# Performance work log

Measured on AMD Instinct MI355X. Metric: run time of the kernel, lower is better.

The kernel has to match this reference:

```python
import jax, jax.numpy as jnp
import numpy as np

B, M, N, C = 8192, 16, 256, 64


def setup_inputs() -> dict:
    key = jax.random.key(0)
    k1, k2 = jax.random.split(key)
    inputs = jax.random.normal(k1, (B, M, C), dtype=jnp.float32)
    codebook = jax.random.normal(k2, (M, N, C), dtype=jnp.float32)
    return {"inputs": inputs, "codebook": codebook}


def reference(inputs, codebook):
    # inputs: [B, M, C]; codebook: [M, N, C]
    # (avoids materializing the torch [B, M, N, C] broadcast difference)
    x2 = jnp.sum(inputs * inputs, axis=-1)[:, :, None]          # [B, M, 1]
    c2 = jnp.sum(codebook * codebook, axis=-1)[None, :, :]      # [1, M, N]
    xc = jnp.einsum('bmc,mnc->bmn', inputs, codebook)           # [B, M, N]
    dist = x2 - 2.0 * xc + c2                                   # [B, M, N]
    idx = jnp.argmin(dist, axis=-1)                             # [B, M] int
    m_idx = jnp.arange(codebook.shape[0])[None, :]              # [1, M]
    codes = codebook[m_idx, idx]                                # [B, M, C]
    return codes, idx
```

## Files before the change

### kernel.cpp

```cpp
#include <hip/hip_runtime.h>
#include <hip/hip_bf16.h>
#include <float.h>


#define BQ 8192
#define MQ 16
#define NQ 256
#define CQ 64
#define RPB 512

typedef short  shortx8 __attribute__((ext_vector_type(8)));
typedef float  f32x4   __attribute__((ext_vector_type(4)));

#define HI_MASK 0xffff0000u

__device__ __forceinline__ void split3_pair(float a, float b,
                                            uint& q0, uint& q1, uint& q2) {
    const uint ba = __builtin_bit_cast(uint, a);
    const uint bb = __builtin_bit_cast(uint, b);
    q0 = (ba >> 16) | (bb & HI_MASK);
    const float r1a = a - __builtin_bit_cast(float, ba & HI_MASK);
    const float r1b = b - __builtin_bit_cast(float, bb & HI_MASK);
    const uint c1a = __builtin_bit_cast(uint, r1a);
    const uint c1b = __builtin_bit_cast(uint, r1b);
    q1 = (c1a >> 16) | (c1b & HI_MASK);
    const float r2a = r1a - __builtin_bit_cast(float, c1a & HI_MASK);
    const float r2b = r1b - __builtin_bit_cast(float, c1b & HI_MASK);
    q2 = (__builtin_bit_cast(uint, r2a) >> 16) |
         (__builtin_bit_cast(uint, r2b) & HI_MASK);
}

__global__ __launch_bounds__(1024, 4) void fq_fused_kernel(
        const float* __restrict__ inputs,
        const float* __restrict__ codebook,
        float* __restrict__ out_codes,
        float* __restrict__ out_idx) {
    const int m    = blockIdx.y;
    const int rowB = blockIdx.x * RPB;
    const int w    = (int)threadIdx.x >> 6;
    const int lane = (int)threadIdx.x & 63;
    const int quad = lane >> 4;
    const int col  = lane & 15;

    __shared__ unsigned short lds_b[96 * 512];
    __shared__ float s_c2v[NQ];

    const float* cbm = codebook + (size_t)m * NQ * CQ;
    #pragma unroll
    for (int it = 0; it < 2; ++it) {
        const int item = (int)threadIdx.x + it * 1024;
        const int kc = item & 7;
        const int n  = item >> 3;
        const int nt = n >> 4, cc = n & 15;
        const int h = kc >> 2, q = kc & 3;
        const float* src = cbm + (size_t)n * CQ + kc * 8;
        const float4 va = *(const float4*)src;
        const float4 vb = *(const float4*)(src + 4);
        const float el[8] = {va.x, va.y, va.z, va.w, vb.x, vb.y, vb.z, vb.w};

        float s = 0.0f;
        #pragma unroll
        for (int u = 0; u < 8; ++u) s = fmaf(el[u], el[u], s);
        s += __shfl_xor(s, 1, 64);
        s += __shfl_xor(s, 2, 64);
        s += __shfl_xor(s, 4, 64);
        if (kc == 0) s_c2v[n] = s;

        uint p0[4], p1[4], p2[4];
        #pragma unroll
        for (int u = 0; u < 4; ++u)
            split3_pair(el[2 * u], el[2 * u + 1], p0[u], p1[u], p2[u]);
        const int lf = q * 16 + cc;
        #pragma unroll
        for (int j = 0; j < 3; ++j) {
            const uint* p = (j == 0) ? p0 : (j == 1) ? p1 : p2;
            unsigned short* dst =
                &lds_b[(((j << 1) + h) * 16 + nt) * 512 + lf * 8];
            *(uint4*)dst = make_uint4(p[0], p[1], p[2], p[3]);
        }
    }
    __syncthreads();

    #pragma unroll 1
    for (int tt = 0; tt < 2; ++tt) {
        const int row0 = rowB + w * 32 + tt * 16;

        const float* xb = inputs + ((size_t)(row0 + col) * MQ + m) * CQ;
        shortx8 afr[3][2];
        #pragma unroll
        for (int h = 0; h < 2; ++h) {
            const float4 va = *(const float4*)(xb + h * 32 + quad * 8);
            const float4 vb = *(const float4*)(xb + h * 32 + quad * 8 + 4);
            const float el[8] = {va.x, va.y, va.z, va.w, vb.x, vb.y, vb.z, vb.w};
            uint q0[4], q1[4], q2[4];
            #pragma unroll
            for (int u = 0; u < 4; ++u)
                split3_pair(el[2 * u], el[2 * u + 1], q0[u], q1[u], q2[u]);
            afr[0][h] = __builtin_bit_cast(shortx8,
                make_uint4(q0[0], q0[1], q0[2], q0[3]));
            afr[1][h] = __builtin_bit_cast(shortx8,
                make_uint4(q1[0], q1[1], q1[2], q1[3]));
            afr[2][h] = __builtin_bit_cast(shortx8,
                make_uint4(q2[0], q2[1], q2[2], q2[3]));
        }

        float bd0[4]; int bi0[4];
        #pragma unroll 1
        for (int chh = 0; chh < 2; ++chh) {
            float c2r[8];
            #pragma unroll
            for (int nt = 0; nt < 8; ++nt)
                c2r[nt] = s_c2v[chh * 128 + nt * 16 + col];

            f32x4 acc[8];
            #pragma unroll
            for (int nt = 0; nt < 8; ++nt)
                acc[nt] = (f32x4){0.f, 0.f, 0.f, 0.f};

            #pragma unroll
            for (int h = 0; h < 2; ++h) {
                #pragma unroll
                for (int j = 0; j < 3; ++j) {
                    shortx8 bfr[8];
                    #pragma unroll
                    for (int nt = 0; nt < 8; ++nt)
                        bfr[nt] = *(const shortx8*)
                            &lds_b[(((j << 1) + h) * 16 + chh * 8 + nt) * 512
                                   + lane * 8];
                    #pragma unroll
                    for (int i = 0; i <= 2 - j; ++i) {
                        #pragma unroll
                        for (int nt = 0; nt < 8; ++nt)
                            acc[nt] = __builtin_amdgcn_mfma_f32_16x16x32_bf16(
                                afr[i][h], bfr[nt], acc[nt], 0, 0, 0);
                    }
                }
            }

            #pragma unroll
            for (int reg = 0; reg < 4; ++reg) {
                float bd = FLT_MAX; int bi = 0;
                #pragma unroll
                for (int nt = 0; nt < 8; ++nt) {
                    const float d = fmaf(-2.0f, acc[nt][reg], c2r[nt]);
                    if (d < bd) { bd = d; bi = chh * 128 + nt * 16 + col; }
                }
                #pragma unroll
                for (int mask = 1; mask <= 8; mask <<= 1) {
                    const float od = __shfl_xor(bd, mask, 64);
                    const int   oi = __shfl_xor(bi, mask, 64);
                    if (od < bd || (od == bd && oi < bi)) { bd = od; bi = oi; }
                }
                if (chh == 0) { bd0[reg] = bd; bi0[reg] = bi; }
                else {
                    if (bd < bd0[reg] || (bd == bd0[reg] && bi < bi0[reg])) {
                        bd0[reg] = bd; bi0[reg] = bi;
                    }
                }
            }
        }

        if (col == 0) {
            #pragma unroll
            for (int reg = 0; reg < 4; ++reg)
                out_idx[(size_t)(row0 + quad * 4 + reg) * MQ + m] =
                    (float)bi0[reg];
        }

        #pragma unroll
        for (int jj = 0; jj < 16; ++jj) {
            const int bn = __shfl(bi0[jj & 3], (jj >> 2) * 16, 64);
            out_codes[((size_t)(row0 + jj) * MQ + m) * CQ + lane] =
                cbm[(size_t)bn * CQ + lane];
        }
    }
}

extern "C" void kernel_launch(void* const* d_in, const int* in_sizes, int n_in,
                              void* d_out, int out_size, void* d_ws, size_t ws_size,
                              hipStream_t stream) {
    const float* inputs   = (const float*)d_in[0];
    const float* codebook = (const float*)d_in[1];
    float* out_codes = (float*)d_out;
    float* out_idx   = (float*)d_out + (size_t)BQ * MQ * CQ;
    (void)d_ws; (void)ws_size;

    fq_fused_kernel<<<dim3(BQ / RPB, MQ), 1024, 0, stream>>>(
        inputs, codebook, out_codes, out_idx);
}
```

Baseline: 108.1 us.

## Process two row tiles per wave to reuse codebook B fragments across MFMAs

Halves the block to 512 threads and has each wave handle two 16-row tiles per iteration, so every codebook fragment read from LDS feeds two MFMA chains. This is meant to cut LDS read traffic per MFMA and raise instruction-level parallelism. In exchange, accumulator and A-fragment registers roughly double, which could lower occupancy, and the codebook prologue loop now runs four times per thread.

```diff
diff --git a/kernel.cpp b/kernel.cpp
--- a/kernel.cpp
+++ b/kernel.cpp
@@ -30,7 +30,7 @@
          (__builtin_bit_cast(uint, r2b) & HI_MASK);
 }
 
-__global__ __launch_bounds__(1024, 4) void fq_fused_kernel(
+__global__ __launch_bounds__(512, 2) void fq_fused_kernel(
         const float* __restrict__ inputs,
         const float* __restrict__ codebook,
         float* __restrict__ out_codes,
@@ -47,8 +47,8 @@
 
     const float* cbm = codebook + (size_t)m * NQ * CQ;
     #pragma unroll
-    for (int it = 0; it < 2; ++it) {
-        const int item = (int)threadIdx.x + it * 1024;
+    for (int it = 0; it < 4; ++it) {
+        const int item = (int)threadIdx.x + it * 512;
         const int kc = item & 7;
         const int n  = item >> 3;
         const int nt = n >> 4, cc = n & 15;
@@ -83,28 +83,33 @@
 
     #pragma unroll 1
     for (int tt = 0; tt < 2; ++tt) {
-        const int row0 = rowB + w * 32 + tt * 16;
-
-        const float* xb = inputs + ((size_t)(row0 + col) * MQ + m) * CQ;
-        shortx8 afr[3][2];
-        #pragma unroll
-        for (int h = 0; h < 2; ++h) {
-            const float4 va = *(const float4*)(xb + h * 32 + quad * 8);
-            const float4 vb = *(const float4*)(xb + h * 32 + quad * 8 + 4);
-            const float el[8] = {va.x, va.y, va.z, va.w, vb.x, vb.y, vb.z, vb.w};
-            uint q0[4], q1[4], q2[4];
-            #pragma unroll
-            for (int u = 0; u < 4; ++u)
-                split3_pair(el[2 * u], el[2 * u + 1], q0[u], q1[u], q2[u]);
-            afr[0][h] = __builtin_bit_cast(shortx8,
-                make_uint4(q0[0], q0[1], q0[2], q0[3]));
-            afr[1][h] = __builtin_bit_cast(shortx8,
-                make_uint4(q1[0], q1[1], q1[2], q1[3]));
-            afr[2][h] = __builtin_bit_cast(shortx8,
-                make_uint4(q2[0], q2[1], q2[2], q2[3]));
-        }
-
-        float bd0[4]; int bi0[4];
+        const int row0 = rowB + w * 64 + tt * 32;
+
+        shortx8 afr[3][2][2];
+        #pragma unroll
+        for (int rt = 0; rt < 2; ++rt) {
+            const float* xb =
+                inputs + ((size_t)(row0 + rt * 16 + col) * MQ + m) * CQ;
+            #pragma unroll
+            for (int h = 0; h < 2; ++h) {
+                const float4 va = *(const float4*)(xb + h * 32 + quad * 8);
+                const float4 vb = *(const float4*)(xb + h * 32 + quad * 8 + 4);
+                const float el[8] = {va.x, va.y, va.z, va.w,
+                                     vb.x, vb.y, vb.z, vb.w};
+                uint q0[4], q1[4], q2[4];
+                #pragma unroll
+                for (int u = 0; u < 4; ++u)
+                    split3_pair(el[2 * u], el[2 * u + 1], q0[u], q1[u], q2[u]);
+                afr[0][rt][h] = __builtin_bit_cast(shortx8,
+                    make_uint4(q0[0], q0[1], q0[2], q0[3]));
+                afr[1][rt][h] = __builtin_bit_cast(shortx8,
+                    make_uint4(q1[0], q1[1], q1[2], q1[3]));
+                afr[2][rt][h] = __builtin_bit_cast(shortx8,
+                    make_uint4(q2[0], q2[1], q2[2], q2[3]));
+            }
+        }
+
+        float bd0[2][4]; int bi0[2][4];
         #pragma unroll 1
         for (int chh = 0; chh < 2; ++chh) {
             float c2r[8];
@@ -112,10 +117,12 @@
             for (int nt = 0; nt < 8; ++nt)
                 c2r[nt] = s_c2v[chh * 128 + nt * 16 + col];
 
-            f32x4 acc[8];
-            #pragma unroll
-            for (int nt = 0; nt < 8; ++nt)
-                acc[nt] = (f32x4){0.f, 0.f, 0.f, 0.f};
+            f32x4 acc[2][8];
+            #pragma unroll
+            for (int rt = 0; rt < 2; ++rt)
+                #pragma unroll
+                for (int nt = 0; nt < 8; ++nt)
+                    acc[rt][nt] = (f32x4){0.f, 0.f, 0.f, 0.f};
 
             #pragma unroll
             for (int h = 0; h < 2; ++h) {
@@ -130,31 +137,38 @@
                     #pragma unroll
                     for (int i = 0; i <= 2 - j; ++i) {
                         #pragma unroll
-                        for (int nt = 0; nt < 8; ++nt)
-                            acc[nt] = __builtin_amdgcn_mfma_f32_16x16x32_bf16(
-                                afr[i][h], bfr[nt], acc[nt], 0, 0, 0);
+                        for (int nt = 0; nt < 8; ++nt) {
+                            acc[0][nt] = __builtin_amdgcn_mfma_f32_16x16x32_bf16(
+                                afr[i][0][h], bfr[nt], acc[0][nt], 0, 0, 0);
+                            acc[1][nt] = __builtin_amdgcn_mfma_f32_16x16x32_bf16(
+                                afr[i][1][h], bfr[nt], acc[1][nt], 0, 0, 0);
+                        }
                     }
                 }
             }
 
             #pragma unroll
-            for (int reg = 0; reg < 4; ++reg) {
-                float bd = FLT_MAX; int bi = 0;
-                #pragma unroll
-                for (int nt = 0; nt < 8; ++nt) {
-                    const float d = fmaf(-2.0f, acc[nt][reg], c2r[nt]);
-                    if (d < bd) { bd = d; bi = chh * 128 + nt * 16 + col; }
-                }
-                #pragma unroll
-                for (int mask = 1; mask <= 8; mask <<= 1) {
-                    const float od = __shfl_xor(bd, mask, 64);
-                    const int   oi = __shfl_xor(bi, mask, 64);
-                    if (od < bd || (od == bd && oi < bi)) { bd = od; bi = oi; }
-                }
-                if (chh == 0) { bd0[reg] = bd; bi0[reg] = bi; }
-                else {
-                    if (bd < bd0[reg] || (bd == bd0[reg] && bi < bi0[reg])) {
-                        bd0[reg] = bd; bi0[reg] = bi;
+            for (int rt = 0; rt < 2; ++rt) {
+                #pragma unroll
+                for (int reg = 0; reg < 4; ++reg) {
+                    float bd = FLT_MAX; int bi = 0;
+                    #pragma unroll
+                    for (int nt = 0; nt < 8; ++nt) {
+                        const float d = fmaf(-2.0f, acc[rt][nt][reg], c2r[nt]);
+                        if (d < bd) { bd = d; bi = chh * 128 + nt * 16 + col; }
+                    }
+                    #pragma unroll
+                    for (int mask = 1; mask <= 8; mask <<= 1) {
+                        const float od = __shfl_xor(bd, mask, 64);
+                        const int   oi = __shfl_xor(bi, mask, 64);
+                        if (od < bd || (od == bd && oi < bi)) { bd = od; bi = oi; }
+                    }
+                    if (chh == 0) { bd0[rt][reg] = bd; bi0[rt][reg] = bi; }
+                    else {
+                        if (bd < bd0[rt][reg] ||
+                            (bd == bd0[rt][reg] && bi < bi0[rt][reg])) {
+                            bd0[rt][reg] = bd; bi0[rt][reg] = bi;
+                        }
                     }
                 }
             }
@@ -162,14 +176,18 @@
 
         if (col == 0) {
             #pragma unroll
-            for (int reg = 0; reg < 4; ++reg)
-                out_idx[(size_t)(row0 + quad * 4 + reg) * MQ + m] =
-                    (float)bi0[reg];
-        }
-
-        #pragma unroll
-        for (int jj = 0; jj < 16; ++jj) {
-            const int bn = __shfl(bi0[jj & 3], (jj >> 2) * 16, 64);
+            for (int rt = 0; rt < 2; ++rt)
+                #pragma unroll
+                for (int reg = 0; reg < 4; ++reg)
+                    out_idx[(size_t)(row0 + rt * 16 + quad * 4 + reg) * MQ + m] =
+                        (float)bi0[rt][reg];
+        }
+
+        #pragma unroll
+        for (int jj = 0; jj < 32; ++jj) {
+            const int rt  = jj >> 4;
+            const int r16 = jj & 15;
+            const int bn  = __shfl(bi0[rt][r16 & 3], (r16 >> 2) * 16, 64);
             out_codes[((size_t)(row0 + jj) * MQ + m) * CQ + lane] =
                 cbm[(size_t)bn * CQ + lane];
         }
@@ -185,6 +203,6 @@
     float* out_idx   = (float*)d_out + (size_t)BQ * MQ * CQ;
     (void)d_ws; (void)ws_size;
 
-    fq_fused_kernel<<<dim3(BQ / RPB, MQ), 1024, 0, stream>>>(
+    fq_fused_kernel<<<dim3(BQ / RPB, MQ), 512, 0, stream>>>(
         inputs, codebook, out_codes, out_idx);
 }
```

New measurement: 113.7 us. 5.1% more time.
